# Performance work log

Measured on AMD Instinct MI355X. Metric: run time of the kernel, lower is better.

Reference implementation:

```python
import jax, jax.numpy as jnp
import numpy as np

B, IN_DIM, OUT_DIM, NNZ = 4096, 9000, 2048, 200000


def setup_inputs() -> dict:
    key = jax.random.key(0)
    k_x, k_r, k_c, k_w, k_b = jax.random.split(key, 5)
    x = jax.random.normal(k_x, (B, IN_DIM), dtype=jnp.float32)
    rows = jax.random.randint(k_r, (NNZ,), 0, IN_DIM, dtype=jnp.int64)
    cols = jax.random.randint(k_c, (NNZ,), 0, OUT_DIM, dtype=jnp.int64)
    nonzero_indices = jnp.stack([rows, cols], axis=1)  # [NNZ, 2]
    weights = jax.random.normal(k_w, (NNZ,), dtype=jnp.float32)
    bias = jax.random.normal(k_b, (OUT_DIM,), dtype=jnp.float32) * 0.1
    return {"x": x, "nonzero_indices": nonzero_indices, "weights": weights, "bias": bias}


def reference(x, nonzero_indices, weights, bias):
    # scatter_nd: build dense [IN_DIM, OUT_DIM] weight matrix from sparse entries
    # (additive semantics, matching tf/torch scatter_nd for duplicate indices)
    W = jnp.zeros((IN_DIM, OUT_DIM), dtype=weights.dtype)
    W = W.at[nonzero_indices[:, 0], nonzero_indices[:, 1]].add(weights)
    # dense mm + bias
    return x @ W + bias
```

## Files before the change

kernel.cpp:

```cpp
#include <hip/hip_runtime.h>

#define B_DIM   4096
#define IN_DIM  9000
#define OUT_DIM 2048
#define NNZ     200000

#define BTILE   128
#define B_TILES (B_DIM / BTILE)
#define COLT_N  64
#define CPB     (OUT_DIM / COLT_N)
#define THREADS 1024
#define NWAVE   (THREADS / 64)

#define FB_BTILE  8
#define FB_SEGLEN 1360
#define FB_NSEG   7
#define FB_NKEY   (FB_NSEG * OUT_DIM)
#define FB_XPAD   12


__global__ void hist_c_kernel(const int* __restrict__ idx, int* __restrict__ cnt) {
    int i = blockIdx.x * blockDim.x + threadIdx.x;
    if (i >= NNZ) return;
    int r = idx[2 * i];
    int c = idx[2 * i + 1];
    if ((unsigned)r < IN_DIM && (unsigned)c < OUT_DIM)
        atomicAdd(&cnt[c], 1);
}

__global__ __launch_bounds__(1024) void scan2048_kernel(const int* __restrict__ cnt,
                                                        int* __restrict__ ks) {
    __shared__ int p[1024];
    int t = threadIdx.x;
    int v0 = cnt[2 * t], v1 = cnt[2 * t + 1];
    p[t] = v0 + v1;
    __syncthreads();
    for (int off = 1; off < 1024; off <<= 1) {
        int v = (t >= off) ? p[t - off] : 0;
        __syncthreads();
        p[t] += v;
        __syncthreads();
    }
    int base = (t == 0) ? 0 : p[t - 1];
    ks[2 * t]     = base;
    ks[2 * t + 1] = base + v0;
    if (t == 1023) ks[2048] = p[1023];
}

__global__ void scatter_c_kernel(const int* __restrict__ idx,
                                 const float* __restrict__ w,
                                 const int* __restrict__ ks,
                                 int* __restrict__ cur,
                                 uint2* __restrict__ entries) {
    int i = blockIdx.x * blockDim.x + threadIdx.x;
    if (i >= NNZ) return;
    int r = idx[2 * i];
    int c = idx[2 * i + 1];
    if ((unsigned)r < IN_DIM && (unsigned)c < OUT_DIM) {
        int pos = ks[c] + atomicAdd(&cur[c], 1);
        entries[pos] = make_uint2((unsigned)r * (B_DIM / 2), __float_as_uint(w[i]));
    }
}

__global__ __launch_bounds__(256) void transpose_kernel(const float* __restrict__ x,
                                                        unsigned short* __restrict__ xT) {
    __shared__ float tile[64][65];
    int r0 = blockIdx.x * 64;
    int b0 = blockIdx.y * 64;
    int t = threadIdx.x;
    {
        int i0 = t >> 6, j = t & 63;
        int r = r0 + j;
#pragma unroll
        for (int ii = 0; ii < 16; ++ii) {
            int i = i0 + 4 * ii;
            tile[i][j] = (r < IN_DIM) ? x[(size_t)(b0 + i) * IN_DIM + r] : 0.f;
        }
    }
    __syncthreads();
    {
        int j0 = t >> 6, i = t & 63;
#pragma unroll
        for (int k = 0; k < 16; ++k) {
            int jr = j0 + 4 * k;
            int r = r0 + jr;
            if (r < IN_DIM) {
                unsigned int u = __float_as_uint(tile[i][jr]);
                unsigned short h =
                    (unsigned short)((u + 0x7fffu + ((u >> 16) & 1u)) >> 16);
                xT[(size_t)r * B_DIM + b0 + i] = h;
            }
        }
    }
}

__global__ __launch_bounds__(THREADS) void spmm_xt_kernel(
    const unsigned int* __restrict__ xTu,
    const float*        __restrict__ bias,
    const int*          __restrict__ ks,
    const uint2*        __restrict__ entries,
    float* __restrict__ out) {

    __shared__ float oacc[CPB * BTILE];
    __shared__ int ctr;

    const int t = threadIdx.x;
    const int lane = t & 63;

    if (t == 0) ctr = 0;
    __syncthreads();

    const int bid = blockIdx.x;
    const int xcd    = bid & 7;
    const int colT   = (bid >> 3) & 63;
    const int group  = bid >> 9;
    const int b_tile = group * 8 + xcd;

    const int laneoff = b_tile * (BTILE / 2) + lane;

    for (;;) {
        int colv = 0;
        if (lane == 0) colv = atomicAdd(&ctr, 1);
        colv = __shfl(colv, 0);
        if (colv >= CPB) break;
        const int col = __builtin_amdgcn_readfirstlane(colv);
        const int c = colT * CPB + col;
        const int s = __builtin_amdgcn_readfirstlane(ks[c]);
        const int e = __builtin_amdgcn_readfirstlane(ks[c + 1]);

        float A0[8], A1[8];
#pragma unroll
        for (int k = 0; k < 8; ++k) { A0[k] = 0.f; A1[k] = 0.f; }

        int jj = s;
        for (; jj + 8 <= e; jj += 8) {
            uint2 E[8];
#pragma unroll
            for (int k = 0; k < 8; ++k) E[k] = entries[jj + k];
            unsigned int u[8];
#pragma unroll
            for (int k = 0; k < 8; ++k) u[k] = xTu[E[k].x + laneoff];
#pragma unroll
            for (int k = 0; k < 8; ++k) {
                float wv = __uint_as_float(E[k].y);
                A0[k] = fmaf(wv, __uint_as_float(u[k] << 16), A0[k]);
                A1[k] = fmaf(wv, __uint_as_float(u[k] & 0xffff0000u), A1[k]);
            }
        }
        if (jj + 4 <= e) {
            uint2 E[4];
#pragma unroll
            for (int k = 0; k < 4; ++k) E[k] = entries[jj + k];
            unsigned int u[4];
#pragma unroll
            for (int k = 0; k < 4; ++k) u[k] = xTu[E[k].x + laneoff];
#pragma unroll
            for (int k = 0; k < 4; ++k) {
                float wv = __uint_as_float(E[k].y);
                A0[k] = fmaf(wv, __uint_as_float(u[k] << 16), A0[k]);
                A1[k] = fmaf(wv, __uint_as_float(u[k] & 0xffff0000u), A1[k]);
            }
            jj += 4;
        }
        for (; jj < e; ++jj) {
            uint2 E0 = entries[jj];
            unsigned int u0 = xTu[E0.x + laneoff];
            float wv = __uint_as_float(E0.y);
            A0[0] = fmaf(wv, __uint_as_float(u0 << 16), A0[0]);
            A1[0] = fmaf(wv, __uint_as_float(u0 & 0xffff0000u), A1[0]);
        }

        float s0 = ((A0[0] + A0[1]) + (A0[2] + A0[3])) +
                   ((A0[4] + A0[5]) + (A0[6] + A0[7]));
        float s1 = ((A1[0] + A1[1]) + (A1[2] + A1[3])) +
                   ((A1[4] + A1[5]) + (A1[6] + A1[7]));

        const int bl0 = 2 * lane;
        oacc[col * BTILE + (bl0 ^ (col & 31))]       = s0;
        oacc[col * BTILE + ((bl0 + 1) ^ (col & 31))] = s1;
    }
    __syncthreads();

    const int tc = t & 31;
    const int tb = t >> 5;
    const int C0 = colT * CPB;
    const size_t B0 = (size_t)b_tile * BTILE;
    const float bi = bias[C0 + tc];
#pragma unroll
    for (int bl = 0; bl < BTILE / 32; ++bl) {
        int b = tb + 32 * bl;
        out[(B0 + b) * OUT_DIM + C0 + tc] = oacc[tc * BTILE + (b ^ (tc & 31))] + bi;
    }
}


__global__ void fb_hist_kernel(const int* __restrict__ idx, int* __restrict__ cnt) {
    int i = blockIdx.x * blockDim.x + threadIdx.x;
    if (i >= NNZ) return;
    int r = idx[2 * i];
    int c = idx[2 * i + 1];
    if ((unsigned)r < IN_DIM && (unsigned)c < OUT_DIM) {
        int seg = r / FB_SEGLEN;
        atomicAdd(&cnt[seg * OUT_DIM + c], 1);
    }
}

__global__ __launch_bounds__(1024) void fb_scan_kernel(const int* __restrict__ cnt,
                                                       int* __restrict__ key_start) {
    __shared__ int lds_c[FB_NKEY];
    __shared__ int lds_p[1024];
    int t = threadIdx.x;
    for (int i = t; i < FB_NKEY; i += 1024) lds_c[i] = cnt[i];
    __syncthreads();
    const int CH = FB_NKEY / 1024;
    int base = t * CH;
    int partial = 0;
    for (int i = 0; i < CH; ++i) partial += lds_c[base + i];
    lds_p[t] = partial;
    __syncthreads();
    for (int off = 1; off < 1024; off <<= 1) {
        int v = (t >= off) ? lds_p[t - off] : 0;
        __syncthreads();
        lds_p[t] += v;
        __syncthreads();
    }
    int run = (t == 0) ? 0 : lds_p[t - 1];
    for (int i = 0; i < CH; ++i) { key_start[base + i] = run; run += lds_c[base + i]; }
    if (t == 1023) key_start[FB_NKEY] = lds_p[1023];
}

__global__ void fb_scatter_kernel(const int* __restrict__ idx,
                                  const float* __restrict__ w,
                                  const int* __restrict__ key_start,
                                  int* __restrict__ cur,
                                  uint2* __restrict__ entries) {
    int i = blockIdx.x * blockDim.x + threadIdx.x;
    if (i >= NNZ) return;
    int r = idx[2 * i];
    int c = idx[2 * i + 1];
    if ((unsigned)r < IN_DIM && (unsigned)c < OUT_DIM) {
        int seg = r / FB_SEGLEN;
        int key = seg * OUT_DIM + c;
        int pos = key_start[key] + atomicAdd(&cur[key], 1);
        entries[pos] = make_uint2((unsigned)(r - seg * FB_SEGLEN), __float_as_uint(w[i]));
    }
}

__global__ __launch_bounds__(1024, 8) void fb_spmm_kernel(
    const float* __restrict__ x,
    const float* __restrict__ bias,
    const int*   __restrict__ key_start,
    const uint2* __restrict__ entries,
    float* __restrict__ out) {

    __shared__ float xs[FB_SEGLEN * FB_XPAD];
    const int t = threadIdx.x;
    const size_t b0 = (size_t)blockIdx.x * FB_BTILE;
    const int c0 = t;
    const int c1 = t + 1024;

    float acc0[FB_BTILE], acc1[FB_BTILE];
#pragma unroll
    for (int b = 0; b < FB_BTILE; ++b) { acc0[b] = 0.f; acc1[b] = 0.f; }

    for (int seg = 0; seg < FB_NSEG; ++seg) {
        const int rbase = seg * FB_SEGLEN;
        const int rlen = (IN_DIM - rbase < FB_SEGLEN) ? (IN_DIM - rbase) : FB_SEGLEN;
        __syncthreads();
#pragma unroll
        for (int b = 0; b < FB_BTILE; ++b) {
            const float* __restrict__ src = x + (b0 + b) * IN_DIM + rbase;
            for (int r = t; r < rlen; r += 1024) xs[r * FB_XPAD + b] = src[r];
        }
        __syncthreads();
        for (int cc = 0; cc < 2; ++cc) {
            int c = cc ? c1 : c0;
            float* acc = cc ? acc1 : acc0;
            int s = key_start[seg * OUT_DIM + c];
            int e = key_start[seg * OUT_DIM + c + 1];
            for (int j = s; j < e; ++j) {
                uint2 en = entries[j];
                float wv = __uint_as_float(en.y);
                const float4* xr = (const float4*)(xs + en.x * FB_XPAD);
                float4 lo = xr[0];
                float4 hi = xr[1];
                acc[0] = fmaf(wv, lo.x, acc[0]);
                acc[1] = fmaf(wv, lo.y, acc[1]);
                acc[2] = fmaf(wv, lo.z, acc[2]);
                acc[3] = fmaf(wv, lo.w, acc[3]);
                acc[4] = fmaf(wv, hi.x, acc[4]);
                acc[5] = fmaf(wv, hi.y, acc[5]);
                acc[6] = fmaf(wv, hi.z, acc[6]);
                acc[7] = fmaf(wv, hi.w, acc[7]);
            }
        }
    }
    const float bi0 = bias[c0];
    const float bi1 = bias[c1];
#pragma unroll
    for (int b = 0; b < FB_BTILE; ++b) {
        out[(b0 + b) * OUT_DIM + c0] = acc0[b] + bi0;
        out[(b0 + b) * OUT_DIM + c1] = acc1[b] + bi1;
    }
}


extern "C" void kernel_launch(void* const* d_in, const int* in_sizes, int n_in,
                              void* d_out, int out_size, void* d_ws, size_t ws_size,
                              hipStream_t stream) {
    const float* x    = (const float*)d_in[0];
    const int*   idx  = (const int*)  d_in[1];
    const float* w    = (const float*)d_in[2];
    const float* bias = (const float*)d_in[3];
    float* out = (float*)d_out;

    const size_t xT_bytes  = (size_t)IN_DIM * B_DIM * 2;
    const size_t int_bytes = ((size_t)(2048 + 2048 + 2049) * 4 + 15) & ~(size_t)15;
    const size_t need = xT_bytes + int_bytes + (size_t)NNZ * 8;

    if (ws_size >= need) {
        unsigned short* xT = (unsigned short*)d_ws;
        int* cnt      = (int*)((char*)d_ws + xT_bytes);
        int* cur      = cnt + 2048;
        int* ks       = cur + 2048;
        uint2* entries = (uint2*)((char*)d_ws + xT_bytes + int_bytes);

        hipMemsetAsync(cnt, 0, 2 * 2048 * sizeof(int), stream);
        hist_c_kernel<<<(NNZ + 255) / 256, 256, 0, stream>>>(idx, cnt);
        scan2048_kernel<<<1, 1024, 0, stream>>>(cnt, ks);
        scatter_c_kernel<<<(NNZ + 255) / 256, 256, 0, stream>>>(idx, w, ks, cur, entries);
        dim3 tg((IN_DIM + 63) / 64, B_DIM / 64);
        transpose_kernel<<<tg, 256, 0, stream>>>(x, xT);
        spmm_xt_kernel<<<B_TILES * COLT_N, THREADS, 0, stream>>>(
            (const unsigned int*)xT, bias, ks, entries, out);
    } else {
        int* cnt       = (int*)d_ws;
        int* cur       = cnt + FB_NKEY;
        int* key_start = cur + FB_NKEY;
        size_t ent_off = ((size_t)(3 * FB_NKEY + 1) * sizeof(int) + 15) & ~(size_t)15;
        uint2* entries = (uint2*)((char*)d_ws + ent_off);

        hipMemsetAsync(cnt, 0, 2 * FB_NKEY * sizeof(int), stream);
        fb_hist_kernel<<<(NNZ + 255) / 256, 256, 0, stream>>>(idx, cnt);
        fb_scan_kernel<<<1, 1024, 0, stream>>>(cnt, key_start);
        fb_scatter_kernel<<<(NNZ + 255) / 256, 256, 0, stream>>>(idx, w, key_start, cur, entries);
        fb_spmm_kernel<<<B_DIM / FB_BTILE, 1024, 0, stream>>>(x, bias, key_start, entries, out);
    }
}
```

Before: 218.0 us.

## Vectorize transpose I/O and software-pipeline sparse gather loop in spmm

The transpose kernel now reads x with float4 loads on full tiles and writes packed pairs of bf16 values as 32-bit words instead of 16-bit stores. The spmm inner loop is restructured into a software pipeline that prefetches entries two batches ahead and gathers one batch ahead, so index loads overlap with FMAs. The separate 4-entry tail step is removed. A launch-bounds occupancy hint of 8 is added, which may force register limits and cause spills given the larger live state.

```diff
diff --git a/kernel.cpp b/kernel.cpp
--- a/kernel.cpp
+++ b/kernel.cpp
@@ -63,12 +63,25 @@
 }
 
 __global__ __launch_bounds__(256) void transpose_kernel(const float* __restrict__ x,
-                                                        unsigned short* __restrict__ xT) {
+                                                        unsigned int* __restrict__ xTu) {
     __shared__ float tile[64][65];
     int r0 = blockIdx.x * 64;
     int b0 = blockIdx.y * 64;
     int t = threadIdx.x;
-    {
+
+    if (r0 + 64 <= IN_DIM) {
+        int j4 = (t & 15) * 4;
+        int i0 = t >> 4;
+#pragma unroll
+        for (int p = 0; p < 4; ++p) {
+            int i = i0 + 16 * p;
+            float4 v = *(const float4*)&x[(size_t)(b0 + i) * IN_DIM + r0 + j4];
+            tile[i][j4 + 0] = v.x;
+            tile[i][j4 + 1] = v.y;
+            tile[i][j4 + 2] = v.z;
+            tile[i][j4 + 3] = v.w;
+        }
+    } else {
         int i0 = t >> 6, j = t & 63;
         int r = r0 + j;
 #pragma unroll
@@ -79,22 +92,24 @@
     }
     __syncthreads();
     {
-        int j0 = t >> 6, i = t & 63;
-#pragma unroll
-        for (int k = 0; k < 16; ++k) {
-            int jr = j0 + 4 * k;
+        int m  = t & 31;
+        int j0 = t >> 5;
+#pragma unroll
+        for (int p = 0; p < 8; ++p) {
+            int jr = j0 + 8 * p;
             int r = r0 + jr;
             if (r < IN_DIM) {
-                unsigned int u = __float_as_uint(tile[i][jr]);
-                unsigned short h =
-                    (unsigned short)((u + 0x7fffu + ((u >> 16) & 1u)) >> 16);
-                xT[(size_t)r * B_DIM + b0 + i] = h;
-            }
-        }
-    }
-}
-
-__global__ __launch_bounds__(THREADS) void spmm_xt_kernel(
+                unsigned int a = __float_as_uint(tile[2 * m][jr]);
+                unsigned int b = __float_as_uint(tile[2 * m + 1][jr]);
+                unsigned int ha = (a + 0x7fffu + ((a >> 16) & 1u)) >> 16;
+                unsigned int hb = (b + 0x7fffu + ((b >> 16) & 1u)) & 0xffff0000u;
+                xTu[(size_t)r * (B_DIM / 2) + (b0 >> 1) + m] = ha | hb;
+            }
+        }
+    }
+}
+
+__global__ __launch_bounds__(THREADS, 8) void spmm_xt_kernel(
     const unsigned int* __restrict__ xTu,
     const float*        __restrict__ bias,
     const int*          __restrict__ ks,
@@ -133,34 +148,67 @@
         for (int k = 0; k < 8; ++k) { A0[k] = 0.f; A1[k] = 0.f; }
 
         int jj = s;
-        for (; jj + 8 <= e; jj += 8) {
-            uint2 E[8];
-#pragma unroll
-            for (int k = 0; k < 8; ++k) E[k] = entries[jj + k];
-            unsigned int u[8];
-#pragma unroll
-            for (int k = 0; k < 8; ++k) u[k] = xTu[E[k].x + laneoff];
+        const int nfull = (e - s) >> 3;
+
+        if (nfull >= 2) {
+            uint2 Ea[8], Eb[8];
+            unsigned int ua[8];
+#pragma unroll
+            for (int k = 0; k < 8; ++k) Ea[k] = entries[jj + k];
+#pragma unroll
+            for (int k = 0; k < 8; ++k) Eb[k] = entries[jj + 8 + k];
+#pragma unroll
+            for (int k = 0; k < 8; ++k) ua[k] = xTu[Ea[k].x + laneoff];
+
+            for (int ib = 0; ib < nfull - 2; ++ib) {
+                uint2 Ec[8];
+#pragma unroll
+                for (int k = 0; k < 8; ++k) Ec[k] = entries[jj + 16 + k];
+                unsigned int ub[8];
+#pragma unroll
+                for (int k = 0; k < 8; ++k) ub[k] = xTu[Eb[k].x + laneoff];
+#pragma unroll
+                for (int k = 0; k < 8; ++k) {
+                    float wv = __uint_as_float(Ea[k].y);
+                    A0[k] = fmaf(wv, __uint_as_float(ua[k] << 16), A0[k]);
+                    A1[k] = fmaf(wv, __uint_as_float(ua[k] & 0xffff0000u), A1[k]);
+                }
+#pragma unroll
+                for (int k = 0; k < 8; ++k) { Ea[k] = Eb[k]; Eb[k] = Ec[k]; ua[k] = ub[k]; }
+                jj += 8;
+            }
+            {
+                unsigned int ub[8];
+#pragma unroll
+                for (int k = 0; k < 8; ++k) ub[k] = xTu[Eb[k].x + laneoff];
+#pragma unroll
+                for (int k = 0; k < 8; ++k) {
+                    float wv = __uint_as_float(Ea[k].y);
+                    A0[k] = fmaf(wv, __uint_as_float(ua[k] << 16), A0[k]);
+                    A1[k] = fmaf(wv, __uint_as_float(ua[k] & 0xffff0000u), A1[k]);
+                }
+#pragma unroll
+                for (int k = 0; k < 8; ++k) {
+                    float wv = __uint_as_float(Eb[k].y);
+                    A0[k] = fmaf(wv, __uint_as_float(ub[k] << 16), A0[k]);
+                    A1[k] = fmaf(wv, __uint_as_float(ub[k] & 0xffff0000u), A1[k]);
+                }
+                jj += 16;
+            }
+        } else if (nfull == 1) {
+            uint2 Ea[8];
+            unsigned int ua[8];
+#pragma unroll
+            for (int k = 0; k < 8; ++k) Ea[k] = entries[jj + k];
+#pragma unroll
+            for (int k = 0; k < 8; ++k) ua[k] = xTu[Ea[k].x + laneoff];
 #pragma unroll
             for (int k = 0; k < 8; ++k) {
-                float wv = __uint_as_float(E[k].y);
-                A0[k] = fmaf(wv, __uint_as_float(u[k] << 16), A0[k]);
-                A1[k] = fmaf(wv, __uint_as_float(u[k] & 0xffff0000u), A1[k]);
-            }
-        }
-        if (jj + 4 <= e) {
-            uint2 E[4];
-#pragma unroll
-            for (int k = 0; k < 4; ++k) E[k] = entries[jj + k];
-            unsigned int u[4];
-#pragma unroll
-            for (int k = 0; k < 4; ++k) u[k] = xTu[E[k].x + laneoff];
-#pragma unroll
-            for (int k = 0; k < 4; ++k) {
-                float wv = __uint_as_float(E[k].y);
-                A0[k] = fmaf(wv, __uint_as_float(u[k] << 16), A0[k]);
-                A1[k] = fmaf(wv, __uint_as_float(u[k] & 0xffff0000u), A1[k]);
-            }
-            jj += 4;
+                float wv = __uint_as_float(Ea[k].y);
+                A0[k] = fmaf(wv, __uint_as_float(ua[k] << 16), A0[k]);
+                A1[k] = fmaf(wv, __uint_as_float(ua[k] & 0xffff0000u), A1[k]);
+            }
+            jj += 8;
         }
         for (; jj < e; ++jj) {
             uint2 E0 = entries[jj];
@@ -319,7 +367,7 @@
     const size_t need = xT_bytes + int_bytes + (size_t)NNZ * 8;
 
     if (ws_size >= need) {
-        unsigned short* xT = (unsigned short*)d_ws;
+        unsigned int* xTu = (unsigned int*)d_ws;
         int* cnt      = (int*)((char*)d_ws + xT_bytes);
         int* cur      = cnt + 2048;
         int* ks       = cur + 2048;
@@ -330,9 +378,9 @@
         scan2048_kernel<<<1, 1024, 0, stream>>>(cnt, ks);
         scatter_c_kernel<<<(NNZ + 255) / 256, 256, 0, stream>>>(idx, w, ks, cur, entries);
         dim3 tg((IN_DIM + 63) / 64, B_DIM / 64);
-        transpose_kernel<<<tg, 256, 0, stream>>>(x, xT);
+        transpose_kernel<<<tg, 256, 0, stream>>>(x, xTu);
         spmm_xt_kernel<<<B_TILES * COLT_N, THREADS, 0, stream>>>(
-            (const unsigned int*)xT, bias, ks, entries, out);
+            xTu, bias, ks, entries, out);
     } else {
         int* cnt       = (int*)d_ws;
         int* cur       = cnt + FB_NKEY;
```

Result: faster. 211.7 us (-2.9%).
